# Optimization experiments

Measured on AMD Instinct MI355X. Metric: run time of the kernel, lower is better.

Reference implementation:

```python
import jax, jax.numpy as jnp
import numpy as np

B, S, C = 4, 2048, 1024

def setup_inputs() -> dict:
    key = jax.random.key(0)
    ks = jax.random.split(key, 9)
    lim = 1.0 / np.sqrt(C)  # torch nn.Linear default init range
    def lin_params(kw, kb):
        W = jax.random.uniform(kw, (C, C), jnp.float32, -lim, lim)
        b = jax.random.uniform(kb, (C,), jnp.float32, -lim, lim)
        return W, b
    Wq, bq = lin_params(ks[0], ks[1])
    Wk, bk = lin_params(ks[2], ks[3])
    Wv, bv = lin_params(ks[4], ks[5])
    query = jax.random.normal(ks[6], (B, S, C), jnp.float32)
    key_t = jax.random.normal(ks[7], (B, S, C), jnp.float32)
    value = jax.random.normal(ks[8], (B, S, C), jnp.float32)
    return {"query": query, "key": key_t, "value": value,
            "Wq": Wq, "bq": bq, "Wk": Wk, "bk": bk, "Wv": Wv, "bv": bv}

def reference(query, key, value, Wq, bq, Wk, bk, Wv, bv):
    # Linear projections: y = x @ W^T + b (torch Linear convention, W is [out, in])
    Q = jnp.einsum('bsc,dc->bsd', query, Wq) + bq
    K = jnp.einsum('bsc,dc->bsd', key, Wk) + bk
    V = jnp.einsum('bsc,dc->bsd', value, Wv) + bv
    scale = jnp.float32(C) ** 0.5
    scores = jnp.einsum('bqd,bkd->bqk', Q, K) / scale  # [B, S, S]
    attn = jax.nn.softmax(scores, axis=-1)
    out = jnp.einsum('bqk,bkd->bqd', attn, V)  # [B, S, C]
    return out
```

## Files before the change

### kernel.cpp

```cpp
#include <hip/hip_runtime.h>
#include <hip/hip_bf16.h>


typedef _Float16 half8 __attribute__((ext_vector_type(8)));
typedef float f32x4 __attribute__((ext_vector_type(4)));

#define AS1(p) ((const __attribute__((address_space(1))) void*)(p))
#define AS3(p) ((__attribute__((address_space(3))) void*)(p))

__global__ __launch_bounds__(256) void cvt3_f32_f16(
    const float* __restrict__ s0, const float* __restrict__ s1,
    const float* __restrict__ s2, _Float16* __restrict__ d0,
    _Float16* __restrict__ d1, _Float16* __restrict__ d2, int n) {
    const float* s = blockIdx.y == 0 ? s0 : blockIdx.y == 1 ? s1 : s2;
    _Float16* d = blockIdx.y == 0 ? d0 : blockIdx.y == 1 ? d1 : d2;
    int i = (blockIdx.x * 256 + threadIdx.x) * 8;
    if (i >= n) return;
    float4 a = *(const float4*)(s + i);
    float4 b = *(const float4*)(s + i + 4);
    half8 h;
    h[0] = (_Float16)a.x; h[1] = (_Float16)a.y; h[2] = (_Float16)a.z; h[3] = (_Float16)a.w;
    h[4] = (_Float16)b.x; h[5] = (_Float16)b.y; h[6] = (_Float16)b.z; h[7] = (_Float16)b.w;
    *(half8*)(d + i) = h;
}

template <int K, bool BIAS, bool F16OUT, int GXS, int GYS, int R>
__global__ __launch_bounds__(256, 2)
void gemm_nt(const _Float16* __restrict__ A, const _Float16* __restrict__ Bt,
             const float* __restrict__ bias, void* __restrict__ Cout,
             int N, float scale, long sA, long sB, long sC) {
    __shared__ _Float16 Asm[128 * 32] __attribute__((aligned(16)));
    __shared__ _Float16 Bsm[128 * 32] __attribute__((aligned(16)));
    const int tid = threadIdx.x;
    const int lane = tid & 63;
    const int wave = tid >> 6;

    const int lin = blockIdx.x;
    const int g = lin & 7;
    const int s = lin >> 3;
    const int xt = s & ((1 << GXS) - 1);
    const int row_id = g * R + (s >> GXS);
    const int yt = row_id & ((1 << GYS) - 1);
    const long zb = row_id >> GYS;
    const int m0 = yt * 128;
    const int n0 = xt * 128;

    A += zb * sA;
    Bt += zb * sB;

    const int srow = lane >> 2;
    const int csw = (((lane & 3) ^ ((srow >> 1) & 3)) << 3);
    const int quad = lane >> 4;
    const int l16 = lane & 15;
    const int aswz = ((quad ^ ((l16 >> 1) & 3)) << 3);
    const int wm = (wave >> 1) << 6;
    const int wn = (wave & 1) << 6;

    f32x4 acc[4][4];
#pragma unroll
    for (int i = 0; i < 4; i++)
#pragma unroll
        for (int j = 0; j < 4; j++)
#pragma unroll
            for (int r = 0; r < 4; r++) acc[i][j][r] = 0.0f;

    const _Float16* Abase = A + (long)m0 * K;
    const _Float16* Bbase = Bt + (long)n0 * K;

    for (int k0 = 0; k0 < K; k0 += 32) {
        __syncthreads();
#pragma unroll
        for (int t = 0; t < 2; ++t) {
            const int rbase = wave * 16 + t * 64;
            __builtin_amdgcn_global_load_lds(
                AS1(Abase + (long)(rbase + srow) * K + k0 + csw),
                AS3(Asm + rbase * 32), 16, 0, 0);
            __builtin_amdgcn_global_load_lds(
                AS1(Bbase + (long)(rbase + srow) * K + k0 + csw),
                AS3(Bsm + rbase * 32), 16, 0, 0);
        }
        __syncthreads();

        half8 af[4], bf[4];
#pragma unroll
        for (int i = 0; i < 4; i++)
            af[i] = *(const half8*)(Asm + (wm + i * 16 + l16) * 32 + aswz);
#pragma unroll
        for (int j = 0; j < 4; j++)
            bf[j] = *(const half8*)(Bsm + (wn + j * 16 + l16) * 32 + aswz);
#pragma unroll
        for (int i = 0; i < 4; i++)
#pragma unroll
            for (int j = 0; j < 4; j++)
                acc[i][j] = __builtin_amdgcn_mfma_f32_16x16x32_f16(af[i], bf[j], acc[i][j], 0, 0, 0);
    }

#pragma unroll
    for (int i = 0; i < 4; i++) {
        const int row = m0 + wm + i * 16 + quad * 4;
#pragma unroll
        for (int j = 0; j < 4; j++) {
            const int col = n0 + wn + j * 16 + l16;
            const float badd = BIAS ? bias[col] : 0.0f;
#pragma unroll
            for (int r = 0; r < 4; r++) {
                float v = acc[i][j][r] * scale + badd;
                if constexpr (F16OUT) {
                    ((_Float16*)Cout + zb * sC)[(long)(row + r) * N + col] = (_Float16)v;
                } else {
                    ((float*)Cout + zb * sC)[(long)(row + r) * N + col] = v;
                }
            }
        }
    }
}

__global__ __launch_bounds__(256) void transpose_f16(const _Float16* __restrict__ src,
                                                     _Float16* __restrict__ dst,
                                                     int rows, int cols) {
    __shared__ _Float16 tile[64 * 72] __attribute__((aligned(16)));
    const long b = blockIdx.z;
    src += b * (long)rows * cols;
    dst += b * (long)rows * cols;
    const int r0 = blockIdx.y * 64;
    const int c0 = blockIdx.x * 64;
    const int t = threadIdx.x;
#pragma unroll
    for (int it = 0; it < 2; ++it) {
        int c = t + it * 256;
        int rr = c >> 3;
        int cc = (c & 7) << 3;
        *(half8*)&tile[rr * 72 + cc] = *(const half8*)&src[(long)(r0 + rr) * cols + c0 + cc];
    }
    __syncthreads();
#pragma unroll
    for (int it = 0; it < 2; ++it) {
        int c = t + it * 256;
        int d = c >> 3;
        int kc = (c & 7) << 3;
        half8 h;
#pragma unroll
        for (int j = 0; j < 8; j++) h[j] = tile[(kc + j) * 72 + d];
        *(half8*)&dst[(long)(c0 + d) * rows + r0 + kc] = h;
    }
}

__global__ __launch_bounds__(256) void softmax_f16(const _Float16* __restrict__ S,
                                                   _Float16* __restrict__ P) {
    const long row = blockIdx.x;
    const int t = threadIdx.x;
    const int wave = t >> 6, lane = t & 63;
    half8 h = ((const half8*)(S + row * 2048))[t];
    float v[8];
#pragma unroll
    for (int j = 0; j < 8; j++) v[j] = (float)h[j];
    float m = v[0];
#pragma unroll
    for (int j = 1; j < 8; j++) m = fmaxf(m, v[j]);
#pragma unroll
    for (int off = 32; off > 0; off >>= 1) m = fmaxf(m, __shfl_xor(m, off, 64));
    __shared__ float redm[4], reds[4];
    if (lane == 0) redm[wave] = m;
    __syncthreads();
    m = fmaxf(fmaxf(redm[0], redm[1]), fmaxf(redm[2], redm[3]));
    float sum = 0.0f;
#pragma unroll
    for (int j = 0; j < 8; j++) { v[j] = __expf(v[j] - m); sum += v[j]; }
#pragma unroll
    for (int off = 32; off > 0; off >>= 1) sum += __shfl_xor(sum, off, 64);
    if (lane == 0) reds[wave] = sum;
    __syncthreads();
    sum = (reds[0] + reds[1]) + (reds[2] + reds[3]);
    const float inv = 1.0f / sum;
    half8 o;
#pragma unroll
    for (int j = 0; j < 8; j++) o[j] = (_Float16)(v[j] * inv);
    ((half8*)(P + row * 2048))[t] = o;
}

extern "C" void kernel_launch(void* const* d_in, const int* in_sizes, int n_in,
                              void* d_out, int out_size, void* d_ws, size_t ws_size,
                              hipStream_t stream) {
    constexpr int B = 4, S = 2048, C = 1024;
    constexpr long XSZ = (long)B * S * C;
    constexpr long WSZ = (long)C * C;

    const float* query = (const float*)d_in[0];
    const float* key   = (const float*)d_in[1];
    const float* value = (const float*)d_in[2];
    const float* Wq = (const float*)d_in[3];
    const float* bq = (const float*)d_in[4];
    const float* Wk = (const float*)d_in[5];
    const float* bk = (const float*)d_in[6];
    const float* Wv = (const float*)d_in[7];
    const float* bv = (const float*)d_in[8];
    float* out = (float*)d_out;
    char* ws = (char*)d_ws;

    _Float16* Xq  = (_Float16*)(ws + 0);
    _Float16* Xk  = (_Float16*)(ws + XSZ * 2);
    _Float16* Xv  = (_Float16*)(ws + 2 * XSZ * 2);
    _Float16* Wqh = (_Float16*)(ws + 3 * XSZ * 2);
    _Float16* Wkh = (_Float16*)(ws + 3 * XSZ * 2 + WSZ * 2);
    _Float16* Wvh = (_Float16*)(ws + 3 * XSZ * 2 + 2 * WSZ * 2);
    _Float16* Vh  = (_Float16*)(ws + 3 * XSZ * 2 + 3 * WSZ * 2);
    _Float16* scores = (_Float16*)(ws + 0);
    _Float16* Qh  = (_Float16*)(ws + 73400320);
    _Float16* Kh  = (_Float16*)(ws + 73400320 + XSZ * 2);
    _Float16* attn = (_Float16*)(ws + 73400320);
    _Float16* Vt  = (_Float16*)(ws + 106954752);
    if (ws_size < 123731968) return;

    cvt3_f32_f16<<<dim3(XSZ / 2048, 3), 256, 0, stream>>>(query, key, value, Xq, Xk, Xv, (int)XSZ);
    cvt3_f32_f16<<<dim3(WSZ / 2048, 3), 256, 0, stream>>>(Wq, Wk, Wv, Wqh, Wkh, Wvh, (int)WSZ);

    gemm_nt<1024, true, true, 3, 6, 8><<<512, 256, 0, stream>>>(Xq, Wqh, bq, Qh, C, 1.0f, 0, 0, 0);
    gemm_nt<1024, true, true, 3, 6, 8><<<512, 256, 0, stream>>>(Xk, Wkh, bk, Kh, C, 1.0f, 0, 0, 0);
    gemm_nt<1024, true, true, 3, 6, 8><<<512, 256, 0, stream>>>(Xv, Wvh, bv, Vh, C, 1.0f, 0, 0, 0);

    dim3 gtr(C / 64, S / 64, B);
    transpose_f16<<<gtr, 256, 0, stream>>>(Vh, Vt, S, C);

    gemm_nt<1024, false, true, 4, 4, 8><<<1024, 256, 0, stream>>>(
        Qh, Kh, nullptr, scores, S, 0.03125f, (long)S * C, (long)S * C, (long)S * S);

    softmax_f16<<<B * S, 256, 0, stream>>>(scores, attn);

    gemm_nt<2048, false, false, 3, 4, 8><<<512, 256, 0, stream>>>(
        attn, Vt, nullptr, out, C, 1.0f, (long)S * S, (long)C * S, (long)S * C);
}
```

Baseline: 336.9 us.

## Fuse V transpose into projection epilogue and use 128x64 tiles for small GEMMs

The V projection GEMM now writes its output directly in transposed [B, C, S] layout through a half4 store in the epilogue, which removes the separate transpose kernel and the intermediate Vh buffer. The GEMM template gains a configurable N tile (TN). The projection GEMMs and the attn·V GEMM switch to 128x64 tiles, doubling their grid to 1024 blocks so that more blocks are available to fill the GPU's compute units. Smaller tiles lower per-block data reuse and raise the share of load traffic per MFMA, and the transposed epilogue writes are strided across rows.

```diff
diff --git a/kernel.cpp b/kernel.cpp
--- a/kernel.cpp
+++ b/kernel.cpp
@@ -3,6 +3,7 @@
 
 
 typedef _Float16 half8 __attribute__((ext_vector_type(8)));
+typedef _Float16 half4 __attribute__((ext_vector_type(4)));
 typedef float f32x4 __attribute__((ext_vector_type(4)));
 
 #define AS1(p) ((const __attribute__((address_space(1))) void*)(p))
@@ -24,13 +25,15 @@
     *(half8*)(d + i) = h;
 }
 
-template <int K, bool BIAS, bool F16OUT, int GXS, int GYS, int R>
+template <int K, int TN, bool BIAS, bool F16OUT, bool TROUT, int GYS>
 __global__ __launch_bounds__(256, 2)
 void gemm_nt(const _Float16* __restrict__ A, const _Float16* __restrict__ Bt,
              const float* __restrict__ bias, void* __restrict__ Cout,
              int N, float scale, long sA, long sB, long sC) {
+    constexpr int JN = TN / 32;
+    constexpr int SLABS = (128 + TN) / 16;
     __shared__ _Float16 Asm[128 * 32] __attribute__((aligned(16)));
-    __shared__ _Float16 Bsm[128 * 32] __attribute__((aligned(16)));
+    __shared__ _Float16 Bsm[TN * 32] __attribute__((aligned(16)));
     const int tid = threadIdx.x;
     const int lane = tid & 63;
     const int wave = tid >> 6;
@@ -38,12 +41,12 @@
     const int lin = blockIdx.x;
     const int g = lin & 7;
     const int s = lin >> 3;
-    const int xt = s & ((1 << GXS) - 1);
-    const int row_id = g * R + (s >> GXS);
+    const int xt = s & 15;
+    const int row_id = g * 8 + (s >> 4);
     const int yt = row_id & ((1 << GYS) - 1);
     const long zb = row_id >> GYS;
     const int m0 = yt * 128;
-    const int n0 = xt * 128;
+    const int n0 = xt * TN;
 
     A += zb * sA;
     Bt += zb * sB;
@@ -54,13 +57,13 @@
     const int l16 = lane & 15;
     const int aswz = ((quad ^ ((l16 >> 1) & 3)) << 3);
     const int wm = (wave >> 1) << 6;
-    const int wn = (wave & 1) << 6;
-
-    f32x4 acc[4][4];
+    const int wn = (wave & 1) * (TN >> 1);
+
+    f32x4 acc[4][JN];
 #pragma unroll
     for (int i = 0; i < 4; i++)
 #pragma unroll
-        for (int j = 0; j < 4; j++)
+        for (int j = 0; j < JN; j++)
 #pragma unroll
             for (int r = 0; r < 4; r++) acc[i][j][r] = 0.0f;
 
@@ -70,28 +73,30 @@
     for (int k0 = 0; k0 < K; k0 += 32) {
         __syncthreads();
 #pragma unroll
-        for (int t = 0; t < 2; ++t) {
-            const int rbase = wave * 16 + t * 64;
-            __builtin_amdgcn_global_load_lds(
-                AS1(Abase + (long)(rbase + srow) * K + k0 + csw),
-                AS3(Asm + rbase * 32), 16, 0, 0);
-            __builtin_amdgcn_global_load_lds(
-                AS1(Bbase + (long)(rbase + srow) * K + k0 + csw),
-                AS3(Bsm + rbase * 32), 16, 0, 0);
+        for (int t = wave; t < SLABS; t += 4) {
+            if (t < 8) {
+                __builtin_amdgcn_global_load_lds(
+                    AS1(Abase + (long)(t * 16 + srow) * K + k0 + csw),
+                    AS3(Asm + t * 512), 16, 0, 0);
+            } else {
+                __builtin_amdgcn_global_load_lds(
+                    AS1(Bbase + (long)((t - 8) * 16 + srow) * K + k0 + csw),
+                    AS3(Bsm + (t - 8) * 512), 16, 0, 0);
+            }
         }
         __syncthreads();
 
-        half8 af[4], bf[4];
+        half8 af[4], bf[JN];
 #pragma unroll
         for (int i = 0; i < 4; i++)
             af[i] = *(const half8*)(Asm + (wm + i * 16 + l16) * 32 + aswz);
 #pragma unroll
-        for (int j = 0; j < 4; j++)
+        for (int j = 0; j < JN; j++)
             bf[j] = *(const half8*)(Bsm + (wn + j * 16 + l16) * 32 + aswz);
 #pragma unroll
         for (int i = 0; i < 4; i++)
 #pragma unroll
-            for (int j = 0; j < 4; j++)
+            for (int j = 0; j < JN; j++)
                 acc[i][j] = __builtin_amdgcn_mfma_f32_16x16x32_f16(af[i], bf[j], acc[i][j], 0, 0, 0);
     }
 
@@ -99,49 +104,28 @@
     for (int i = 0; i < 4; i++) {
         const int row = m0 + wm + i * 16 + quad * 4;
 #pragma unroll
-        for (int j = 0; j < 4; j++) {
+        for (int j = 0; j < JN; j++) {
             const int col = n0 + wn + j * 16 + l16;
             const float badd = BIAS ? bias[col] : 0.0f;
-#pragma unroll
-            for (int r = 0; r < 4; r++) {
-                float v = acc[i][j][r] * scale + badd;
-                if constexpr (F16OUT) {
-                    ((_Float16*)Cout + zb * sC)[(long)(row + r) * N + col] = (_Float16)v;
-                } else {
-                    ((float*)Cout + zb * sC)[(long)(row + r) * N + col] = v;
+            if constexpr (TROUT) {
+                const long b = row >> 11;
+                const int sl = row & 2047;
+                half4 h;
+#pragma unroll
+                for (int r = 0; r < 4; r++) h[r] = (_Float16)(acc[i][j][r] * scale + badd);
+                *(half4*)((_Float16*)Cout + b * 2097152 + (long)col * 2048 + sl) = h;
+            } else {
+#pragma unroll
+                for (int r = 0; r < 4; r++) {
+                    float v = acc[i][j][r] * scale + badd;
+                    if constexpr (F16OUT) {
+                        ((_Float16*)Cout + zb * sC)[(long)(row + r) * N + col] = (_Float16)v;
+                    } else {
+                        ((float*)Cout + zb * sC)[(long)(row + r) * N + col] = v;
+                    }
                 }
             }
         }
-    }
-}
-
-__global__ __launch_bounds__(256) void transpose_f16(const _Float16* __restrict__ src,
-                                                     _Float16* __restrict__ dst,
-                                                     int rows, int cols) {
-    __shared__ _Float16 tile[64 * 72] __attribute__((aligned(16)));
-    const long b = blockIdx.z;
-    src += b * (long)rows * cols;
-    dst += b * (long)rows * cols;
-    const int r0 = blockIdx.y * 64;
-    const int c0 = blockIdx.x * 64;
-    const int t = threadIdx.x;
-#pragma unroll
-    for (int it = 0; it < 2; ++it) {
-        int c = t + it * 256;
-        int rr = c >> 3;
-        int cc = (c & 7) << 3;
-        *(half8*)&tile[rr * 72 + cc] = *(const half8*)&src[(long)(r0 + rr) * cols + c0 + cc];
-    }
-    __syncthreads();
-#pragma unroll
-    for (int it = 0; it < 2; ++it) {
-        int c = t + it * 256;
-        int d = c >> 3;
-        int kc = (c & 7) << 3;
-        half8 h;
-#pragma unroll
-        for (int j = 0; j < 8; j++) h[j] = tile[(kc + j) * 72 + d];
-        *(half8*)&dst[(long)(c0 + d) * rows + r0 + kc] = h;
     }
 }
 
@@ -203,7 +187,6 @@
     _Float16* Wqh = (_Float16*)(ws + 3 * XSZ * 2);
     _Float16* Wkh = (_Float16*)(ws + 3 * XSZ * 2 + WSZ * 2);
     _Float16* Wvh = (_Float16*)(ws + 3 * XSZ * 2 + 2 * WSZ * 2);
-    _Float16* Vh  = (_Float16*)(ws + 3 * XSZ * 2 + 3 * WSZ * 2);
     _Float16* scores = (_Float16*)(ws + 0);
     _Float16* Qh  = (_Float16*)(ws + 73400320);
     _Float16* Kh  = (_Float16*)(ws + 73400320 + XSZ * 2);
@@ -214,18 +197,15 @@
     cvt3_f32_f16<<<dim3(XSZ / 2048, 3), 256, 0, stream>>>(query, key, value, Xq, Xk, Xv, (int)XSZ);
     cvt3_f32_f16<<<dim3(WSZ / 2048, 3), 256, 0, stream>>>(Wq, Wk, Wv, Wqh, Wkh, Wvh, (int)WSZ);
 
-    gemm_nt<1024, true, true, 3, 6, 8><<<512, 256, 0, stream>>>(Xq, Wqh, bq, Qh, C, 1.0f, 0, 0, 0);
-    gemm_nt<1024, true, true, 3, 6, 8><<<512, 256, 0, stream>>>(Xk, Wkh, bk, Kh, C, 1.0f, 0, 0, 0);
-    gemm_nt<1024, true, true, 3, 6, 8><<<512, 256, 0, stream>>>(Xv, Wvh, bv, Vh, C, 1.0f, 0, 0, 0);
-
-    dim3 gtr(C / 64, S / 64, B);
-    transpose_f16<<<gtr, 256, 0, stream>>>(Vh, Vt, S, C);
-
-    gemm_nt<1024, false, true, 4, 4, 8><<<1024, 256, 0, stream>>>(
+    gemm_nt<1024, 64, true, true, false, 6><<<1024, 256, 0, stream>>>(Xq, Wqh, bq, Qh, C, 1.0f, 0, 0, 0);
+    gemm_nt<1024, 64, true, true, false, 6><<<1024, 256, 0, stream>>>(Xk, Wkh, bk, Kh, C, 1.0f, 0, 0, 0);
+    gemm_nt<1024, 64, true, true, true, 6><<<1024, 256, 0, stream>>>(Xv, Wvh, bv, Vt, C, 1.0f, 0, 0, 0);
+
+    gemm_nt<1024, 128, false, true, false, 4><<<1024, 256, 0, stream>>>(
         Qh, Kh, nullptr, scores, S, 0.03125f, (long)S * C, (long)S * C, (long)S * S);
 
     softmax_f16<<<B * S, 256, 0, stream>>>(scores, attn);
 
-    gemm_nt<2048, false, false, 3, 4, 8><<<512, 256, 0, stream>>>(
+    gemm_nt<2048, 64, false, false, false, 4><<<1024, 256, 0, stream>>>(
         attn, Vt, nullptr, out, C, 1.0f, (long)S * S, (long)C * S, (long)S * C);
 }
```

Measured after the change: 353.7 us. +5.0%, slower.
